# Kernel tuning notes

Hardware: AMD Instinct MI355X
Metric: run time of the kernel (lower is better)

The kernel has to match this reference:

```python
import jax, jax.numpy as jnp
import numpy as np
import math

HID = 256      # hidden_dim
POS = 32       # pos_dim (hardcoded num_pos_feats=32 in pos2embed call)
HEADS = 4
DH = HID // HEADS
B = 8          # number of ragged batches
N = 2048       # points per batch (inputs and queries, equal counts)
LN_EPS = 1e-5


def pos2embed(pos, num_pos_feats=POS):
    # pos: [..., 3] -> [..., 3*num_pos_feats]; faithfully keeps the original
    # bug where pos_z's cos half uses pos_x.
    pos = pos * (2.0 * math.pi)
    dim_t = jnp.arange(num_pos_feats, dtype=jnp.float32)
    dim_t = 2.0 * jnp.floor(dim_t / 2.0) / num_pos_feats + 1.0
    px = pos[..., 0, None] / dim_t
    py = pos[..., 1, None] / dim_t
    pz = pos[..., 2, None] / dim_t
    def interleave(s, c):
        return jnp.stack((s, c), axis=-1).reshape(*s.shape[:-1], -1)
    ex = interleave(jnp.sin(px[..., 0::2]), jnp.cos(px[..., 1::2]))
    ey = interleave(jnp.sin(py[..., 0::2]), jnp.cos(py[..., 1::2]))
    ez = interleave(jnp.sin(pz[..., 0::2]), jnp.cos(px[..., 1::2]))  # original bug
    return jnp.concatenate((ey, ex, ez), axis=-1)


def setup_inputs() -> dict:
    key = jax.random.key(0)
    ks = jax.random.split(key, 16)
    inputs = jax.random.normal(ks[0], (B * N, HID), jnp.float32)
    Q_in = jax.random.normal(ks[1], (B * N, HID), jnp.float32)
    bid = jnp.repeat(jnp.arange(B, dtype=jnp.float32), N)[:, None]
    input_coords = jnp.concatenate([bid, jax.random.uniform(ks[2], (B * N, 3), jnp.float32)], -1)
    Q_in_coords = jnp.concatenate([bid, jax.random.uniform(ks[3], (B * N, 3), jnp.float32)], -1)
    s = 0.02
    Wq = jax.random.normal(ks[4], (HID, HID + POS), jnp.float32) * s
    Wk = jax.random.normal(ks[5], (HID, HID + POS), jnp.float32) * s
    Wv = jax.random.normal(ks[6], (HID, HID + POS), jnp.float32) * s
    in_proj_w = jax.random.normal(ks[7], (3 * HID, HID), jnp.float32) * s
    in_proj_b = jnp.zeros((3 * HID,), jnp.float32)
    out_proj_w = jax.random.normal(ks[8], (HID, HID), jnp.float32) * s
    out_proj_b = jnp.zeros((HID,), jnp.float32)
    ln_g = jnp.ones((HID,), jnp.float32)
    ln_b = jnp.zeros((HID,), jnp.float32)
    pe_w1 = jax.random.normal(ks[9], (POS, POS * 3), jnp.float32) * s
    pe_b1 = jnp.zeros((POS,), jnp.float32)
    pe_w2 = jax.random.normal(ks[10], (POS, POS), jnp.float32) * s
    pe_b2 = jnp.zeros((POS,), jnp.float32)
    return dict(inputs=inputs, Q_in=Q_in, input_coords=input_coords, Q_in_coords=Q_in_coords,
                Wq=Wq, Wk=Wk, Wv=Wv, in_proj_w=in_proj_w, in_proj_b=in_proj_b,
                out_proj_w=out_proj_w, out_proj_b=out_proj_b, ln_g=ln_g, ln_b=ln_b,
                pe_w1=pe_w1, pe_b1=pe_b1, pe_w2=pe_w2, pe_b2=pe_b2)


def reference(inputs, Q_in, input_coords, Q_in_coords, Wq, Wk, Wv,
              in_proj_w, in_proj_b, out_proj_w, out_proj_b, ln_g, ln_b,
              pe_w1, pe_b1, pe_w2, pe_b2):
    # Equal per-batch counts let the ragged per-batch loop be one batched op.
    def pos_mlp(coords):  # [BN,4] -> [B,N,POS]
        e = pos2embed(coords[:, 1:], POS)                   # [BN, 3*POS]
        h = jax.nn.relu(e @ pe_w1.T + pe_b1)
        return (h @ pe_w2.T + pe_b2).reshape(B, N, POS)

    xb = inputs.reshape(B, N, HID)
    qb = Q_in.reshape(B, N, HID)
    ip = jnp.concatenate([xb, pos_mlp(input_coords)], -1)   # [B,N,HID+POS]
    qp = jnp.concatenate([qb, pos_mlp(Q_in_coords)], -1)

    Q = jnp.einsum('bnc,hc->bnh', qp, Wq)
    K = jnp.einsum('bnc,hc->bnh', ip, Wk)
    V = jnp.einsum('bnc,hc->bnh', ip, Wv)

    # nn.MultiheadAttention: its own in_proj on top of Q/K/V, then out_proj
    wq, wk, wv = in_proj_w[:HID], in_proj_w[HID:2 * HID], in_proj_w[2 * HID:]
    bq, bk, bv = in_proj_b[:HID], in_proj_b[HID:2 * HID], in_proj_b[2 * HID:]
    q = (Q @ wq.T + bq).reshape(B, N, HEADS, DH)
    k = (K @ wk.T + bk).reshape(B, N, HEADS, DH)
    v = (V @ wv.T + bv).reshape(B, N, HEADS, DH)

    scores = jnp.einsum('bqhd,bkhd->bhqk', q, k) / math.sqrt(DH)
    attn = jax.nn.softmax(scores, axis=-1)
    o = jnp.einsum('bhqk,bkhd->bqhd', attn, v).reshape(B, N, HID)
    o = o @ out_proj_w.T + out_proj_b

    # residual + LayerNorm (dropout is identity in eval)
    y = qb + o
    mu = y.mean(-1, keepdims=True)
    var = ((y - mu) ** 2).mean(-1, keepdims=True)
    yn = (y - mu) / jnp.sqrt(var + LN_EPS) * ln_g + ln_b
    return yn.reshape(B * N, HID)
```

## Files before the change

kernel.cpp:

```cpp
#include <hip/hip_runtime.h>
#include <math.h>

#define HID 256
#define CIN 288
#define NTOK 16384
#define NSEQ 2048
#define NH 4
#define DHD 64
#define TWO_PI 6.2831853071795864769f

typedef __attribute__((ext_vector_type(8))) short bf16x8;
typedef __attribute__((ext_vector_type(4))) float f32x4;
typedef __attribute__((ext_vector_type(4))) unsigned short u16x4;

__device__ __forceinline__ ushort f2bf(float x) {
    unsigned u = __float_as_uint(x);
    u = (u + 0x7FFFu + ((u >> 16) & 1u)) >> 16;
    return (ushort)u;
}

__device__ __forceinline__ float fast_exp2(float x) {
    return __builtin_amdgcn_exp2f(x);
}

__device__ __forceinline__ unsigned pack_bf_trunc(float a, float b) {
    return __builtin_amdgcn_perm(__float_as_uint(b), __float_as_uint(a), 0x07060302u);
}

__device__ __forceinline__ void gload_lds16(const ushort* g, ushort* l) {
    __builtin_amdgcn_global_load_lds(
        (const __attribute__((address_space(1))) unsigned*)g,
        (__attribute__((address_space(3))) unsigned*)l, 16, 0, 0);
}

__device__ __forceinline__ int sw(int row) {
    return (((row >> 3) << 1) ^ row) & 7;
}

__global__ void fuse_w_kernel(const float* __restrict__ inW,
                              const float* __restrict__ Wq,
                              const float* __restrict__ Wk,
                              const float* __restrict__ Wv,
                              ushort* __restrict__ Wb) {
    __shared__ float wrow[256];
    const int o = blockIdx.x;
    const int mat = blockIdx.y;
    const int t = threadIdx.x;
    if (t < 256) wrow[t] = inW[(mat * 256 + o) * 256 + t];
    __syncthreads();
    if (t >= CIN) return;
    const float* Wm = (mat == 0) ? Wq : ((mat == 1) ? Wk : Wv);
    float acc = 0.f;
#pragma unroll 4
    for (int h = 0; h < 256; ++h) acc += wrow[h] * Wm[h * CIN + t];
    Wb[(size_t)(mat * 256 + o) * CIN + t] = f2bf(acc);
}

__global__ void cast_wo(const float* __restrict__ Wo, ushort* __restrict__ WoB) {
    const int f = (blockIdx.x * 256 + threadIdx.x) * 4;
    const float4 a = *(const float4*)(Wo + f);
    u16x4 o = {f2bf(a.x), f2bf(a.y), f2bf(a.z), f2bf(a.w)};
    *(u16x4*)(WoB + f) = o;
}

__global__ __launch_bounds__(128) void pos_mlp_kernel(
        const float* __restrict__ icoords, const float* __restrict__ qcoords,
        const float* __restrict__ w1, const float* __restrict__ b1,
        const float* __restrict__ w2, const float* __restrict__ b2,
        ushort* __restrict__ ip, ushort* __restrict__ qp) {
    __shared__ float sw1t[96 * 32];
    __shared__ float sb1[32];
    __shared__ float sw2[32 * 32];
    __shared__ float sb2[32];
    const int t = threadIdx.x;
    for (int i = t; i < 96 * 32; i += 128) {
        const int e = i >> 5, r = i & 31;
        sw1t[i] = w1[r * 96 + e];
    }
    for (int i = t; i < 32 * 32; i += 128) sw2[i] = w2[i];
    if (t < 32) { sb1[t] = b1[t]; sb2[t] = b2[t]; }
    __syncthreads();

    const int tok = blockIdx.x * 128 + t;
    const int which = tok >> 14;
    const int m = tok & (NTOK - 1);
    const float* cr = (which ? qcoords : icoords) + m * 4;
    const float x = cr[1] * TWO_PI;
    const float y = cr[2] * TWO_PI;
    const float z = cr[3] * TWO_PI;

    f32x4 h4[8];
#pragma unroll
    for (int r4 = 0; r4 < 8; ++r4) h4[r4] = *(const f32x4*)&sb1[r4 * 4];

    for (int jj = 0; jj < 16; ++jj) {
        const float inv = 1.0f / (1.0f + 0.0625f * (float)jj);
        const float xs = x * inv, ys = y * inv, zs = z * inv;
        const float cx = __cosf(xs);
        float vals[6];
        int idx[6];
        vals[0] = __sinf(ys);  idx[0] = 2 * jj;
        vals[1] = __cosf(ys);  idx[1] = 2 * jj + 1;
        vals[2] = __sinf(xs);  idx[2] = 32 + 2 * jj;
        vals[3] = cx;          idx[3] = 32 + 2 * jj + 1;
        vals[4] = __sinf(zs);  idx[4] = 64 + 2 * jj;
        vals[5] = cx;          idx[5] = 64 + 2 * jj + 1;
#pragma unroll
        for (int u = 0; u < 6; ++u) {
            const float ev = vals[u];
            const f32x4* wr = (const f32x4*)&sw1t[idx[u] * 32];
#pragma unroll
            for (int r4 = 0; r4 < 8; ++r4) h4[r4] += ev * wr[r4];
        }
    }
#pragma unroll
    for (int r4 = 0; r4 < 8; ++r4)
#pragma unroll
        for (int j = 0; j < 4; ++j) h4[r4][j] = fmaxf(h4[r4][j], 0.f);

    ushort* dst = (which ? qp : ip) + (size_t)m * CIN + 256;
#pragma unroll
    for (int c = 0; c < 32; ++c) {
        const f32x4* w4 = (const f32x4*)&sw2[c * 32];
        f32x4 a4 = h4[0] * w4[0];
#pragma unroll
        for (int r4 = 1; r4 < 8; ++r4) a4 += h4[r4] * w4[r4];
        dst[c] = f2bf(sb2[c] + (a4[0] + a4[1]) + (a4[2] + a4[3]));
    }
}

__global__ void cast_x_kernel(const float* __restrict__ X, const float* __restrict__ Qin,
                              ushort* __restrict__ ip, ushort* __restrict__ qp) {
    const int which = blockIdx.y;
    const size_t f = ((size_t)blockIdx.x * 256 + threadIdx.x) * 8;
    const int row = (int)(f >> 8);
    const int col = (int)(f & 255);
    const float* src = which ? Qin : X;
    ushort* dst = which ? qp : ip;
    const float4 a = *(const float4*)(src + f);
    const float4 b = *(const float4*)(src + f + 4);
    u16x4 o0 = {f2bf(a.x), f2bf(a.y), f2bf(a.z), f2bf(a.w)};
    u16x4 o1 = {f2bf(b.x), f2bf(b.y), f2bf(b.z), f2bf(b.w)};
    *(u16x4*)(dst + (size_t)row * CIN + col) = o0;
    *(u16x4*)(dst + (size_t)row * CIN + col + 4) = o1;
}

__global__ __launch_bounds__(256) void qkv_mfma(
        const ushort* __restrict__ qp, const ushort* __restrict__ ip,
        const ushort* __restrict__ Wb, const float* __restrict__ bias,
        ushort* __restrict__ qout, ushort* __restrict__ kout, ushort* __restrict__ vout) {
    __shared__ ushort SA[2 * 4096];
    const int wv = threadIdx.x >> 6, lane = threadIdx.x & 63;
    const int l16 = lane & 15, quad = lane >> 4;
    const int m0b = blockIdx.x * 128;
    const int y = blockIdx.y;
    const int mat = y >> 2;
    const int n0 = y * 64;
    const ushort* A = (mat == 0) ? qp : ip;

    size_t asrc[2];
    int adst[2];
#pragma unroll
    for (int i = 0; i < 2; ++i) {
        const int idx = wv * 128 + i * 64 + lane;
        const int row = idx >> 2, cc = idx & 3;
        asrc[i] = (size_t)(m0b + row) * CIN + cc * 8;
        adst[i] = (wv * 128 + i * 64) * 8;
    }
    int aoff[2];
#pragma unroll
    for (int s = 0; s < 2; ++s)
        aoff[s] = ((32 * wv + 16 * s + l16) * 4 + quad) * 8;

    f32x4 acc[2][4];
#pragma unroll
    for (int s = 0; s < 2; ++s)
#pragma unroll
        for (int c = 0; c < 4; ++c) acc[s][c] = (f32x4){0.f, 0.f, 0.f, 0.f};

#pragma unroll
    for (int i = 0; i < 2; ++i)
        gload_lds16(A + asrc[i], SA + adst[i]);

    for (int t = 0; t < 9; ++t) {
        __syncthreads();
        if (t + 1 < 9) {
            const int bo = ((t + 1) & 1) * 4096;
#pragma unroll
            for (int i = 0; i < 2; ++i)
                gload_lds16(A + asrc[i] + (t + 1) * 32, SA + bo + adst[i]);
        }
        const ushort* buf = SA + (t & 1) * 4096;
        const int kk = t * 32;
        bf16x8 af[2], bf[4];
#pragma unroll
        for (int s = 0; s < 2; ++s)
            af[s] = *(const bf16x8*)(buf + aoff[s]);
#pragma unroll
        for (int c = 0; c < 4; ++c)
            bf[c] = *(const bf16x8*)(Wb + (size_t)(n0 + 16 * c + l16) * CIN + kk + quad * 8);
        if (mat < 2) {
#pragma unroll
            for (int s = 0; s < 2; ++s)
#pragma unroll
                for (int c = 0; c < 4; ++c)
                    acc[s][c] = __builtin_amdgcn_mfma_f32_16x16x32_bf16(bf[c], af[s], acc[s][c], 0, 0, 0);
        } else {
#pragma unroll
            for (int s = 0; s < 2; ++s)
#pragma unroll
                for (int c = 0; c < 4; ++c)
                    acc[s][c] = __builtin_amdgcn_mfma_f32_16x16x32_bf16(af[s], bf[c], acc[s][c], 0, 0, 0);
        }
    }

    const int h = y & 3;
    const int m0 = m0b + wv * 32;
    if (mat < 2) {
        const float scale = (mat == 0) ? (0.125f * 1.44269504088896f) : 1.0f;
        ushort* out = (mat == 0) ? qout : kout;
#pragma unroll
        for (int s = 0; s < 2; ++s) {
            const int tokm = m0 + 16 * s + l16;
            const int b = tokm >> 11, nn = tokm & (NSEQ - 1);
#pragma unroll
            for (int c = 0; c < 4; ++c) {
                const f32x4 b4 = *(const f32x4*)&bias[n0 + 16 * c + quad * 4];
                u16x4 w;
#pragma unroll
                for (int r = 0; r < 4; ++r) w[r] = f2bf((acc[s][c][r] + b4[r]) * scale);
                *(u16x4*)(out + ((size_t)(b * NH + h) * NSEQ + nn) * DHD + 16 * c + quad * 4) = w;
            }
        }
    } else {
#pragma unroll
        for (int s = 0; s < 2; ++s) {
            const int tok0 = m0 + 16 * s + quad * 4;
            const int b = tok0 >> 11, nn0 = tok0 & (NSEQ - 1);
#pragma unroll
            for (int c = 0; c < 4; ++c) {
                const int d = 16 * c + l16;
                const float bv = bias[n0 + d];
                u16x4 w;
#pragma unroll
                for (int r = 0; r < 4; ++r) w[r] = f2bf(acc[s][c][r] + bv);
                *(u16x4*)(vout + ((size_t)(b * NH + h) * DHD + d) * NSEQ + nn0) = w;
            }
        }
    }
}

__global__ __launch_bounds__(256) void attn_kernel(
        const ushort* __restrict__ q, const ushort* __restrict__ k,
        const ushort* __restrict__ v, ushort* __restrict__ out) {
    __shared__ ushort SL[2 * 8192];
    const int bh = blockIdx.y;
    const int wv = threadIdx.x >> 6;
    const int lane = threadIdx.x & 63;
    const int l16 = lane & 15, quad = lane >> 4;
    const int q0 = blockIdx.x * 128 + wv * 32;

    const ushort* qb = q + (size_t)bh * NSEQ * DHD;
    const ushort* kb = k + (size_t)bh * NSEQ * DHD;
    const ushort* vb = v + (size_t)bh * DHD * NSEQ;

    bf16x8 qf[2][2];
#pragma unroll
    for (int s = 0; s < 2; ++s)
#pragma unroll
        for (int hh = 0; hh < 2; ++hh)
            qf[s][hh] = *(const bf16x8*)(qb + (size_t)(q0 + 16 * s + l16) * DHD + 32 * hh + quad * 8);

    int ksrc[2], vsrc[2], sdst[2];
#pragma unroll
    for (int i = 0; i < 2; ++i) {
        const int idx = wv * 128 + i * 64 + lane;
        const int row = idx >> 3;
        const int cg = (idx & 7) ^ sw(row);
        ksrc[i] = row * DHD + cg * 8;
        vsrc[i] = row * NSEQ + cg * 8;
        sdst[i] = (wv * 128 + i * 64) * 8;
    }

    const int krow = 8 * (l16 >> 2) + (l16 & 3);
    int koff[2][2][2];
    int voff[2][4];
#pragma unroll
    for (int sub = 0; sub < 2; ++sub) {
#pragma unroll
        for (int m = 0; m < 2; ++m) {
            const int row = sub * 32 + krow + 4 * m;
#pragma unroll
            for (int hh = 0; hh < 2; ++hh)
                koff[sub][m][hh] = (row * 8 + ((hh * 4 + quad) ^ sw(row))) * 8;
        }
#pragma unroll
        for (int c = 0; c < 4; ++c) {
            const int row = 16 * c + l16;
            voff[sub][c] = 4096 + (row * 8 + ((sub * 4 + quad) ^ sw(row))) * 8;
        }
    }

    f32x4 Oc[2][4];
#pragma unroll
    for (int s = 0; s < 2; ++s)
#pragma unroll
        for (int c = 0; c < 4; ++c) Oc[s][c] = (f32x4){0.f, 0.f, 0.f, 0.f};
    float lrun[2] = {0.f, 0.f};

#pragma unroll
    for (int i = 0; i < 2; ++i) {
        gload_lds16(kb + ksrc[i], SL + sdst[i]);
        gload_lds16(vb + vsrc[i], SL + 4096 + sdst[i]);
    }

    for (int t = 0; t < 32; ++t) {
        __syncthreads();
        if (t + 1 < 32) {
            const int bo = ((t + 1) & 1) * 8192;
            const int kt = (t + 1) * 64;
#pragma unroll
            for (int i = 0; i < 2; ++i) {
                gload_lds16(kb + (size_t)kt * DHD + ksrc[i], SL + bo + sdst[i]);
                gload_lds16(vb + kt + vsrc[i], SL + bo + 4096 + sdst[i]);
            }
        }
        const ushort* buf = SL + (t & 1) * 8192;

#pragma unroll
        for (int sub = 0; sub < 2; ++sub) {
            bf16x8 kf[2][2], vf[4];
#pragma unroll
            for (int m = 0; m < 2; ++m)
#pragma unroll
                for (int hh = 0; hh < 2; ++hh)
                    kf[m][hh] = *(const bf16x8*)(buf + koff[sub][m][hh]);
#pragma unroll
            for (int c = 0; c < 4; ++c)
                vf[c] = *(const bf16x8*)(buf + voff[sub][c]);

#pragma unroll
            for (int s = 0; s < 2; ++s) {
                f32x4 s0 = (f32x4){0.f, 0.f, 0.f, 0.f};
                f32x4 s1 = (f32x4){0.f, 0.f, 0.f, 0.f};
                s0 = __builtin_amdgcn_mfma_f32_16x16x32_bf16(kf[0][0], qf[s][0], s0, 0, 0, 0);
                s0 = __builtin_amdgcn_mfma_f32_16x16x32_bf16(kf[0][1], qf[s][1], s0, 0, 0, 0);
                s1 = __builtin_amdgcn_mfma_f32_16x16x32_bf16(kf[1][0], qf[s][0], s1, 0, 0, 0);
                s1 = __builtin_amdgcn_mfma_f32_16x16x32_bf16(kf[1][1], qf[s][1], s1, 0, 0, 0);

                float p0[4], p1[4];
#pragma unroll
                for (int r = 0; r < 4; ++r) {
                    p0[r] = fast_exp2(s0[r]);
                    p1[r] = fast_exp2(s1[r]);
                }
                lrun[s] += (p0[0] + p0[1]) + (p0[2] + p0[3]) + (p1[0] + p1[1]) + (p1[2] + p1[3]);

                union { bf16x8 v8; unsigned d[4]; } P;
                P.d[0] = pack_bf_trunc(p0[0], p0[1]);
                P.d[1] = pack_bf_trunc(p0[2], p0[3]);
                P.d[2] = pack_bf_trunc(p1[0], p1[1]);
                P.d[3] = pack_bf_trunc(p1[2], p1[3]);
#pragma unroll
                for (int c = 0; c < 4; ++c)
                    Oc[s][c] = __builtin_amdgcn_mfma_f32_16x16x32_bf16(vf[c], P.v8, Oc[s][c], 0, 0, 0);
            }
        }
    }

    const int b = bh >> 2, h = bh & 3;
#pragma unroll
    for (int s = 0; s < 2; ++s) {
        float ls = lrun[s];
        ls += __shfl_xor(ls, 16);
        ls += __shfl_xor(ls, 32);
        const float linv = 1.0f / ls;
        ushort* dst = out + (size_t)(b * NSEQ + q0 + 16 * s + l16) * HID + h * DHD;
#pragma unroll
        for (int c = 0; c < 4; ++c) {
            u16x4 w;
#pragma unroll
            for (int r = 0; r < 4; ++r) w[r] = f2bf(Oc[s][c][r] * linv);
            *(u16x4*)(dst + 16 * c + quad * 4) = w;
        }
    }
}

__global__ __launch_bounds__(256) void oproj_ln_mfma(
        const ushort* __restrict__ abuf, const float* __restrict__ Qin,
        const ushort* __restrict__ WoB, const float* __restrict__ bo,
        const float* __restrict__ g, const float* __restrict__ be,
        float* __restrict__ out) {
    __shared__ float yt[32][260];
    const int wv = threadIdx.x >> 6, lane = threadIdx.x & 63;
    const int l16 = lane & 15, quad = lane >> 4;
    const int m0 = blockIdx.x * 32;
    const int n0 = wv * 64;

    f32x4 acc[2][4];
#pragma unroll
    for (int s = 0; s < 2; ++s)
#pragma unroll
        for (int c = 0; c < 4; ++c) acc[s][c] = (f32x4){0.f, 0.f, 0.f, 0.f};

    for (int kk = 0; kk < HID; kk += 32) {
        bf16x8 af[2], bf[4];
#pragma unroll
        for (int s = 0; s < 2; ++s)
            af[s] = *(const bf16x8*)(abuf + (size_t)(m0 + 16 * s + l16) * HID + kk + quad * 8);
#pragma unroll
        for (int c = 0; c < 4; ++c)
            bf[c] = *(const bf16x8*)(WoB + (size_t)(n0 + 16 * c + l16) * HID + kk + quad * 8);
#pragma unroll
        for (int s = 0; s < 2; ++s)
#pragma unroll
            for (int c = 0; c < 4; ++c)
                acc[s][c] = __builtin_amdgcn_mfma_f32_16x16x32_bf16(af[s], bf[c], acc[s][c], 0, 0, 0);
    }

#pragma unroll
    for (int s = 0; s < 2; ++s)
#pragma unroll
        for (int c = 0; c < 4; ++c) {
            const int col = n0 + 16 * c + l16;
            const float bv = bo[col];
#pragma unroll
            for (int r = 0; r < 4; ++r) {
                const int row = 16 * s + quad * 4 + r;
                yt[row][col] = acc[s][c][r] + bv + Qin[(size_t)(m0 + row) * HID + col];
            }
        }
    __syncthreads();

    float gv[4], bev[4];
#pragma unroll
    for (int u = 0; u < 4; ++u) { gv[u] = g[lane + 64 * u]; bev[u] = be[lane + 64 * u]; }

    for (int rr = 0; rr < 8; ++rr) {
        const int row = wv * 8 + rr;
        float sm = 0.f, ssq = 0.f;
        float yv[4];
#pragma unroll
        for (int u = 0; u < 4; ++u) {
            yv[u] = yt[row][lane + 64 * u];
            sm += yv[u]; ssq += yv[u] * yv[u];
        }
#pragma unroll
        for (int off = 32; off >= 1; off >>= 1) {
            sm += __shfl_xor(sm, off);
            ssq += __shfl_xor(ssq, off);
        }
        const float mu = sm * (1.f / 256.f);
        const float rs = rsqrtf(fmaxf(ssq * (1.f / 256.f) - mu * mu, 0.f) + 1e-5f);
        float* dst = out + (size_t)(m0 + row) * HID;
#pragma unroll
        for (int u = 0; u < 4; ++u)
            dst[lane + 64 * u] = (yv[u] - mu) * rs * gv[u] + bev[u];
    }
}

extern "C" void kernel_launch(void* const* d_in, const int* in_sizes, int n_in,
                              void* d_out, int out_size, void* d_ws, size_t ws_size,
                              hipStream_t stream) {
    const float* inputs       = (const float*)d_in[0];
    const float* Q_in         = (const float*)d_in[1];
    const float* input_coords = (const float*)d_in[2];
    const float* Q_in_coords  = (const float*)d_in[3];
    const float* Wq           = (const float*)d_in[4];
    const float* Wk           = (const float*)d_in[5];
    const float* Wv           = (const float*)d_in[6];
    const float* in_proj_w    = (const float*)d_in[7];
    const float* in_proj_b    = (const float*)d_in[8];
    const float* out_proj_w   = (const float*)d_in[9];
    const float* out_proj_b   = (const float*)d_in[10];
    const float* ln_g         = (const float*)d_in[11];
    const float* ln_b         = (const float*)d_in[12];
    const float* pe_w1        = (const float*)d_in[13];
    const float* pe_b1        = (const float*)d_in[14];
    const float* pe_w2        = (const float*)d_in[15];
    const float* pe_b2        = (const float*)d_in[16];

    char* ws = (char*)d_ws;
    ushort* Wb   = (ushort*)(ws);
    ushort* WoB  = (ushort*)(ws + 442368);
    ushort* qp   = (ushort*)(ws + 573440);
    ushort* ip   = (ushort*)(ws + 10010624);
    ushort* qbuf = (ushort*)(ws + 19447808);
    ushort* kbuf = (ushort*)(ws + 27836416);
    ushort* vbuf = (ushort*)(ws + 36225024);
    ushort* abuf = (ushort*)(ws + 44613632);

    fuse_w_kernel<<<dim3(256, 3), 320, 0, stream>>>(in_proj_w, Wq, Wk, Wv, Wb);
    cast_wo<<<64, 256, 0, stream>>>(out_proj_w, WoB);
    pos_mlp_kernel<<<256, 128, 0, stream>>>(input_coords, Q_in_coords,
                                            pe_w1, pe_b1, pe_w2, pe_b2, ip, qp);
    cast_x_kernel<<<dim3(2048, 2), 256, 0, stream>>>(inputs, Q_in, ip, qp);
    qkv_mfma<<<dim3(128, 12), 256, 0, stream>>>(qp, ip, Wb, in_proj_b,
                                                qbuf, kbuf, vbuf);
    attn_kernel<<<dim3(16, 32), 256, 0, stream>>>(qbuf, kbuf, vbuf, abuf);
    oproj_ln_mfma<<<512, 256, 0, stream>>>(abuf, Q_in, WoB, out_proj_b,
                                           ln_g, ln_b, (float*)d_out);
}
```

Baseline: 236.1 us.

## Split attention over key halves and merge partial outputs in a normalization kernel

The attention grid gains a third dimension that splits the 2048 keys into two halves, doubling the block count from 512 to 1024 so more CUs are occupied. Each half writes unnormalized bf16 partial outputs and row sums, and a new attn_norm kernel adds the halves and divides by the combined sum. The separate Wo cast kernel is folded into the weight fusion kernel to save a launch. The split works without max rescaling because the softmax apparently uses no running max, but it adds an extra kernel, extra global traffic, and an additional bf16 rounding of the partial outputs.

```diff
diff --git a/kernel.cpp b/kernel.cpp
--- a/kernel.cpp
+++ b/kernel.cpp
@@ -10,6 +10,7 @@
 #define TWO_PI 6.2831853071795864769f
 
 typedef __attribute__((ext_vector_type(8))) short bf16x8;
+typedef __attribute__((ext_vector_type(8))) unsigned short u16x8;
 typedef __attribute__((ext_vector_type(4))) float f32x4;
 typedef __attribute__((ext_vector_type(4))) unsigned short u16x4;
 
@@ -19,6 +20,10 @@
     return (ushort)u;
 }
 
+__device__ __forceinline__ float bf2f(ushort u) {
+    return __uint_as_float((unsigned)u << 16);
+}
+
 __device__ __forceinline__ float fast_exp2(float x) {
     return __builtin_amdgcn_exp2f(x);
 }
@@ -41,11 +46,17 @@
                               const float* __restrict__ Wq,
                               const float* __restrict__ Wk,
                               const float* __restrict__ Wv,
-                              ushort* __restrict__ Wb) {
+                              const float* __restrict__ Wo,
+                              ushort* __restrict__ Wb,
+                              ushort* __restrict__ WoB) {
     __shared__ float wrow[256];
     const int o = blockIdx.x;
     const int mat = blockIdx.y;
     const int t = threadIdx.x;
+    if (mat == 3) {
+        if (t < 256) WoB[o * 256 + t] = f2bf(Wo[o * 256 + t]);
+        return;
+    }
     if (t < 256) wrow[t] = inW[(mat * 256 + o) * 256 + t];
     __syncthreads();
     if (t >= CIN) return;
@@ -54,13 +65,6 @@
 #pragma unroll 4
     for (int h = 0; h < 256; ++h) acc += wrow[h] * Wm[h * CIN + t];
     Wb[(size_t)(mat * 256 + o) * CIN + t] = f2bf(acc);
-}
-
-__global__ void cast_wo(const float* __restrict__ Wo, ushort* __restrict__ WoB) {
-    const int f = (blockIdx.x * 256 + threadIdx.x) * 4;
-    const float4 a = *(const float4*)(Wo + f);
-    u16x4 o = {f2bf(a.x), f2bf(a.y), f2bf(a.z), f2bf(a.w)};
-    *(u16x4*)(WoB + f) = o;
 }
 
 __global__ __launch_bounds__(128) void pos_mlp_kernel(
@@ -252,17 +256,19 @@
 
 __global__ __launch_bounds__(256) void attn_kernel(
         const ushort* __restrict__ q, const ushort* __restrict__ k,
-        const ushort* __restrict__ v, ushort* __restrict__ out) {
+        const ushort* __restrict__ v, ushort* __restrict__ pO,
+        float* __restrict__ lbuf) {
     __shared__ ushort SL[2 * 8192];
     const int bh = blockIdx.y;
+    const int z = blockIdx.z;
     const int wv = threadIdx.x >> 6;
     const int lane = threadIdx.x & 63;
     const int l16 = lane & 15, quad = lane >> 4;
     const int q0 = blockIdx.x * 128 + wv * 32;
 
     const ushort* qb = q + (size_t)bh * NSEQ * DHD;
-    const ushort* kb = k + (size_t)bh * NSEQ * DHD;
-    const ushort* vb = v + (size_t)bh * DHD * NSEQ;
+    const ushort* kb = k + (size_t)bh * NSEQ * DHD + (size_t)z * 1024 * DHD;
+    const ushort* vb = v + (size_t)bh * DHD * NSEQ + z * 1024;
 
     bf16x8 qf[2][2];
 #pragma unroll
@@ -314,9 +320,9 @@
         gload_lds16(vb + vsrc[i], SL + 4096 + sdst[i]);
     }
 
-    for (int t = 0; t < 32; ++t) {
+    for (int t = 0; t < 16; ++t) {
         __syncthreads();
-        if (t + 1 < 32) {
+        if (t + 1 < 16) {
             const int bo = ((t + 1) & 1) * 8192;
             const int kt = (t + 1) * 64;
 #pragma unroll
@@ -369,21 +375,42 @@
     }
 
     const int b = bh >> 2, h = bh & 3;
+    ushort* pOz = pO + (size_t)z * NTOK * HID;
 #pragma unroll
     for (int s = 0; s < 2; ++s) {
         float ls = lrun[s];
         ls += __shfl_xor(ls, 16);
         ls += __shfl_xor(ls, 32);
-        const float linv = 1.0f / ls;
-        ushort* dst = out + (size_t)(b * NSEQ + q0 + 16 * s + l16) * HID + h * DHD;
+        if (quad == 0)
+            lbuf[(size_t)(z * 32 + bh) * NSEQ + q0 + 16 * s + l16] = ls;
+        ushort* dst = pOz + (size_t)(b * NSEQ + q0 + 16 * s + l16) * HID + h * DHD;
 #pragma unroll
         for (int c = 0; c < 4; ++c) {
             u16x4 w;
 #pragma unroll
-            for (int r = 0; r < 4; ++r) w[r] = f2bf(Oc[s][c][r] * linv);
+            for (int r = 0; r < 4; ++r) w[r] = f2bf(Oc[s][c][r]);
             *(u16x4*)(dst + 16 * c + quad * 4) = w;
         }
     }
+}
+
+__global__ __launch_bounds__(256) void attn_norm(
+        const ushort* __restrict__ pO, const float* __restrict__ lbuf,
+        ushort* __restrict__ abuf) {
+    const size_t e = ((size_t)blockIdx.x * 256 + threadIdx.x) * 8;
+    const int tok = (int)(e >> 8);
+    const int c = (int)(e & 255);
+    const int b = tok >> 11, n = tok & (NSEQ - 1);
+    const int bh = b * NH + (c >> 6);
+    const float l = lbuf[(size_t)bh * NSEQ + n] + lbuf[(size_t)(32 + bh) * NSEQ + n];
+    const float linv = 1.0f / l;
+    const u16x8 o0 = *(const u16x8*)(pO + e);
+    const u16x8 o1 = *(const u16x8*)(pO + (size_t)NTOK * HID + e);
+    u16x8 w;
+#pragma unroll
+    for (int j = 0; j < 8; ++j)
+        w[j] = f2bf((bf2f(o0[j]) + bf2f(o1[j])) * linv);
+    *(u16x8*)(abuf + e) = w;
 }
 
 __global__ __launch_bounds__(256) void oproj_ln_mfma(
@@ -489,15 +516,18 @@
     ushort* kbuf = (ushort*)(ws + 27836416);
     ushort* vbuf = (ushort*)(ws + 36225024);
     ushort* abuf = (ushort*)(ws + 44613632);
-
-    fuse_w_kernel<<<dim3(256, 3), 320, 0, stream>>>(in_proj_w, Wq, Wk, Wv, Wb);
-    cast_wo<<<64, 256, 0, stream>>>(out_proj_w, WoB);
+    ushort* pO   = (ushort*)(ws + 53002240);
+    float*  lbuf = (float*) (ws + 69779456);
+
+    fuse_w_kernel<<<dim3(256, 4), 320, 0, stream>>>(in_proj_w, Wq, Wk, Wv,
+                                                    out_proj_w, Wb, WoB);
     pos_mlp_kernel<<<256, 128, 0, stream>>>(input_coords, Q_in_coords,
                                             pe_w1, pe_b1, pe_w2, pe_b2, ip, qp);
     cast_x_kernel<<<dim3(2048, 2), 256, 0, stream>>>(inputs, Q_in, ip, qp);
     qkv_mfma<<<dim3(128, 12), 256, 0, stream>>>(qp, ip, Wb, in_proj_b,
                                                 qbuf, kbuf, vbuf);
-    attn_kernel<<<dim3(16, 32), 256, 0, stream>>>(qbuf, kbuf, vbuf, abuf);
+    attn_kernel<<<dim3(16, 32, 2), 256, 0, stream>>>(qbuf, kbuf, vbuf, pO, lbuf);
+    attn_norm<<<2048, 256, 0, stream>>>(pO, lbuf, abuf);
     oproj_ln_mfma<<<512, 256, 0, stream>>>(abuf, Q_in, WoB, out_proj_b,
                                            ln_g, ln_b, (float*)d_out);
 }
```

Result: no change. 239.4 us (+1.4%).
